# Performance work log

Measured on AMD Instinct MI355X. Metric: run time of the kernel, lower is better.

Reference implementation:

```python
import jax, jax.numpy as jnp
import numpy as np

N = 100000
E = 1600000
D_IN = 64
D_HID = 64
D_OUT = 64


def setup_inputs() -> dict:
    key = jax.random.key(0)
    ks = jax.random.split(key, 12)
    x = jax.random.normal(ks[0], (N, D_IN), dtype=jnp.float32)
    edge_index = jax.random.randint(ks[1], (2, E), 0, N, dtype=jnp.int64)
    s1 = 1.0 / np.sqrt(D_IN)
    s2 = 1.0 / np.sqrt(D_HID)
    return {
        "x": x,
        "edge_index": edge_index,
        "W1l": jax.random.uniform(ks[2], (D_HID, D_IN), jnp.float32, -s1, s1),
        "b1l": jax.random.uniform(ks[3], (D_HID,), jnp.float32, -s1, s1),
        "W1r": jax.random.uniform(ks[4], (D_HID, D_IN), jnp.float32, -s1, s1),
        "W2l": jax.random.uniform(ks[5], (D_HID, D_HID), jnp.float32, -s2, s2),
        "b2l": jax.random.uniform(ks[6], (D_HID,), jnp.float32, -s2, s2),
        "W2r": jax.random.uniform(ks[7], (D_HID, D_HID), jnp.float32, -s2, s2),
        "Wout": jax.random.uniform(ks[8], (D_OUT, D_HID), jnp.float32, -s2, s2),
        "bout": jax.random.uniform(ks[9], (D_OUT,), jnp.float32, -s2, s2),
        "drop": 0,
    }


def _sage_conv(x, src, dst, Wl, bl, Wr, n_nodes):
    # PyG SAGEConv, aggr='mean': out = lin_l(mean_j x_j) + lin_r(x_i)
    msg = x[src]                                            # [E, d] gather
    agg = jax.ops.segment_sum(msg, dst, num_segments=n_nodes)
    deg = jax.ops.segment_sum(jnp.ones((src.shape[0],), x.dtype), dst,
                              num_segments=n_nodes)
    mean = agg / jnp.maximum(deg, 1.0)[:, None]             # empty neighborhoods -> 0
    return mean @ Wl.T + bl + x @ Wr.T


def reference(x, edge_index, W1l, b1l, W1r, W2l, b2l, W2r, Wout, bout, drop):
    src, dst = edge_index[0], edge_index[1]
    n = x.shape[0]
    # dropout is identity in eval mode (training=False); drop unused
    h = jax.nn.relu(_sage_conv(x, src, dst, W1l, b1l, W1r, n))
    h = jax.nn.relu(_sage_conv(h, src, dst, W2l, b2l, W2r, n))
    logits = h @ Wout.T + bout
    return jax.nn.log_softmax(logits, axis=1)
```

## Files before the change

kernel.cpp:

```cpp
#include <hip/hip_runtime.h>


#define TB 256
#define NBINA 256
#define XFB 512
#define CAPB 2560

typedef __attribute__((ext_vector_type(8))) short bf16x8;
typedef __attribute__((ext_vector_type(4))) float f32x4;
typedef __attribute__((ext_vector_type(2))) float f32x2;

__device__ __forceinline__ unsigned short bf16c(float f) {
  union { float f; unsigned u; } v; v.f = f;
  unsigned r = (v.u + 0x7FFFu + ((v.u >> 16) & 1u)) >> 16;
  return (unsigned short)r;
}

__device__ __forceinline__ bf16x8 ld_bf8(const float* p) {
  float4 a = *(const float4*)p;
  float4 b = *(const float4*)(p + 4);
  bf16x8 r;
  r[0] = bf16c(a.x); r[1] = bf16c(a.y); r[2] = bf16c(a.z); r[3] = bf16c(a.w);
  r[4] = bf16c(b.x); r[5] = bf16c(b.y); r[6] = bf16c(b.z); r[7] = bf16c(b.w);
  return r;
}

__device__ __forceinline__ float bflo(unsigned u) { return __uint_as_float(u << 16); }
__device__ __forceinline__ float bfhi(unsigned u) { return __uint_as_float(u & 0xFFFF0000u); }
__device__ __forceinline__ unsigned bfpk(float lo, float hi) {
  return (unsigned)bf16c(lo) | ((unsigned)bf16c(hi) << 16);
}

__global__ __launch_bounds__(256) void k_binA_xf(
    const int* __restrict__ ei, int E,
    int* __restrict__ bucket_fill, unsigned int* __restrict__ bucketData, int NB,
    const float* __restrict__ xin, const float* __restrict__ Wl,
    const float* __restrict__ Wr, const float* __restrict__ bl,
    unsigned short* __restrict__ y, unsigned short* __restrict__ zout, int n) {
  if (blockIdx.x < NBINA) {
    __shared__ int hist[1024];
    __shared__ int base[1024];
    __shared__ int s_nz;
    if (threadIdx.x == 0) s_nz = 0;
    for (int i = threadIdx.x; i < NB; i += TB) hist[i] = 0;
    __syncthreads();
    int nz = 0;
    for (int i = threadIdx.x; i < 2048; i += TB) nz |= ei[2 * i + 1];
    if (nz) atomicOr(&s_nz, 1);
    __syncthreads();
    bool m64 = (s_nz == 0);
    int bb = blockIdx.x;

    long long e0 = (long long)E * bb / NBINA;
    long long e1 = (long long)E * (bb + 1) / NBINA;
    for (long long e = e0 + threadIdx.x; e < e1; e += TB) {
      int dst = m64 ? ((const int2*)ei)[(long long)E + e].x : ei[(long long)E + e];
      atomicAdd(&hist[dst >> 7], 1);
    }
    __syncthreads();
    for (int b = threadIdx.x; b < NB; b += TB) {
      int c = hist[b];
      base[b] = c ? atomicAdd(&bucket_fill[b], c) : 0;
      hist[b] = 0;
    }
    __syncthreads();
    for (long long e = e0 + threadIdx.x; e < e1; e += TB) {
      int src, dst;
      if (m64) {
        src = ((const int2*)ei)[e].x;
        dst = ((const int2*)ei)[(long long)E + e].x;
      } else {
        src = ei[e];
        dst = ei[(long long)E + e];
      }
      int b = dst >> 7;
      int pos = base[b] + atomicAdd(&hist[b], 1);
      if (pos < CAPB)
        bucketData[(size_t)b * CAPB + pos] =
            ((unsigned)(dst & 127) << 24) | (unsigned)src;
    }
    return;
  }

  int lane = threadIdx.x & 63;
  int quad = lane >> 4, m = lane & 15;
  int w0 = ((blockIdx.x - NBINA) * TB + threadIdx.x) >> 6;
  int nw = (XFB * TB) >> 6;

  bf16x8 bfrag[8][2];
  float bias[4];
#pragma unroll
  for (int t = 0; t < 8; ++t) {
    const float* W = (t < 4) ? Wl : Wr;
    int row = (t & 3) * 16 + m;
#pragma unroll
    for (int s = 0; s < 2; ++s)
      bfrag[t][s] = ld_bf8(W + row * 64 + s * 32 + quad * 8);
  }
#pragma unroll
  for (int t = 0; t < 4; ++t) bias[t] = bl[t * 16 + m];

  int nT = (n + 15) >> 4;
  for (int tile = w0; tile < nT; tile += nw) {
    int node0 = tile << 4;
    int mrow = node0 + m;
    if (mrow >= n) mrow = n - 1;
    const float* xr = xin + (size_t)mrow * 64;
    bf16x8 a0 = ld_bf8(xr + quad * 8);
    bf16x8 a1 = ld_bf8(xr + 32 + quad * 8);

    f32x4 acc[8];
#pragma unroll
    for (int t = 0; t < 8; ++t) {
      f32x4 z4 = {0.f, 0.f, 0.f, 0.f};
      z4 = __builtin_amdgcn_mfma_f32_16x16x32_bf16(a0, bfrag[t][0], z4, 0, 0, 0);
      acc[t] = __builtin_amdgcn_mfma_f32_16x16x32_bf16(a1, bfrag[t][1], z4, 0, 0, 0);
    }

#pragma unroll
    for (int r = 0; r < 4; ++r) {
      int node = node0 + quad * 4 + r;
      if (node >= n) break;
      size_t rb = (size_t)node * 64 + m;
#pragma unroll
      for (int t = 0; t < 4; ++t) y[rb + t * 16] = bf16c(acc[t][r]);
#pragma unroll
      for (int t = 0; t < 4; ++t) zout[rb + t * 16] = bf16c(acc[t + 4][r] + bias[t]);
    }
  }
}

__global__ __launch_bounds__(256) void k_binB(
    const unsigned int* __restrict__ bucketData, const int* __restrict__ bucket_fill,
    int* __restrict__ colp, int* __restrict__ cnt) {
  __shared__ unsigned int slice[128 * 64];
  __shared__ int lcnt[128];
  int b = blockIdx.x;
  for (int i = threadIdx.x; i < 128; i += TB) lcnt[i] = 0;
  __syncthreads();
  int fcnt = bucket_fill[b];
  if (fcnt > CAPB) fcnt = CAPB;
  const unsigned int* bd = bucketData + (size_t)b * CAPB;
  for (int k = threadIdx.x; k < fcnt; k += TB) {
    unsigned int rec = bd[k];
    int dl = rec >> 24;
    int pos = atomicAdd(&lcnt[dl], 1);
    if (pos < 64) slice[(dl << 6) + pos] = rec & 0xFFFFFFu;
  }
  __syncthreads();
  size_t obase = (size_t)b * (128 * 64);
  for (int i = threadIdx.x * 4; i < 128 * 64; i += TB * 4) {
    *(uint4*)(colp + obase + i) = *(const uint4*)(slice + i);
  }
  int node0 = b << 7;
  for (int i = threadIdx.x; i < 128; i += TB) cnt[node0 + i] = lcnt[i];
}

__global__ __launch_bounds__(256) void k_xform_b16(
    const unsigned short* zin, const float* __restrict__ Wl,
    const float* __restrict__ Wr, const float* __restrict__ bl,
    unsigned short* __restrict__ y, unsigned short* zout, int n) {
  int lane = threadIdx.x & 63;
  int quad = lane >> 4, m = lane & 15;
  int w0 = (blockIdx.x * blockDim.x + threadIdx.x) >> 6;
  int nw = (gridDim.x * blockDim.x) >> 6;

  bf16x8 bfrag[8][2];
  float bias[4];
#pragma unroll
  for (int t = 0; t < 8; ++t) {
    const float* W = (t < 4) ? Wl : Wr;
    int row = (t & 3) * 16 + m;
#pragma unroll
    for (int s = 0; s < 2; ++s)
      bfrag[t][s] = ld_bf8(W + row * 64 + s * 32 + quad * 8);
  }
#pragma unroll
  for (int t = 0; t < 4; ++t) bias[t] = bl[t * 16 + m];

  int nT = (n + 15) >> 4;
  for (int tile = w0; tile < nT; tile += nw) {
    int node0 = tile << 4;
    int mrow = node0 + m;
    if (mrow >= n) mrow = n - 1;
    const unsigned short* xr = zin + (size_t)mrow * 64;
    bf16x8 a0 = *(const bf16x8*)(xr + quad * 8);
    bf16x8 a1 = *(const bf16x8*)(xr + 32 + quad * 8);

    f32x4 acc[8];
#pragma unroll
    for (int t = 0; t < 8; ++t) {
      f32x4 z4 = {0.f, 0.f, 0.f, 0.f};
      z4 = __builtin_amdgcn_mfma_f32_16x16x32_bf16(a0, bfrag[t][0], z4, 0, 0, 0);
      acc[t] = __builtin_amdgcn_mfma_f32_16x16x32_bf16(a1, bfrag[t][1], z4, 0, 0, 0);
    }

#pragma unroll
    for (int r = 0; r < 4; ++r) {
      int node = node0 + quad * 4 + r;
      if (node >= n) break;
      size_t rb = (size_t)node * 64 + m;
#pragma unroll
      for (int t = 0; t < 4; ++t) y[rb + t * 16] = bf16c(acc[t][r]);
#pragma unroll
      for (int t = 0; t < 4; ++t) zout[rb + t * 16] = bf16c(acc[t + 4][r] + bias[t]);
    }
  }
}

__global__ __launch_bounds__(256) void k_aggr(
    const unsigned short* __restrict__ yb, const int* __restrict__ cnt,
    const int* __restrict__ colp, unsigned short* zio, int n) {
  const unsigned int* y = (const unsigned int*)yb;
  int lane = threadIdx.x & 63;
  int wv = (blockIdx.x * blockDim.x + threadIdx.x) >> 6;
  int g16 = lane & 48;
  int lig = lane & 15;
  int sub = lig >> 3;
  int fo = (lig & 7) * 4;

  int node = (wv << 2) + (g16 >> 4);
  bool act = node < n;
  int cn = act ? node : 0;
  int deg = cnt[cn];
  int jcap = deg < 64 ? deg : 64;
  size_t crow = (size_t)cn << 6;
  int cidxA = colp[crow + lig];
  int cidxB = colp[crow + 16 + lig];

  int wmax = jcap;
  wmax = max(wmax, __shfl_xor(wmax, 16, 64));
  wmax = max(wmax, __shfl_xor(wmax, 32, 64));

  f32x2 acc[4];
#pragma unroll
  for (int k = 0; k < 4; ++k) acc[k] = (f32x2){0.f, 0.f};

#define ACCUM(U)                                             \
  do {                                                       \
    acc[0] += (f32x2){bflo((U).x), bfhi((U).x)};             \
    acc[1] += (f32x2){bflo((U).y), bfhi((U).y)};             \
    acc[2] += (f32x2){bflo((U).z), bfhi((U).z)};             \
    acc[3] += (f32x2){bflo((U).w), bfhi((U).w)};             \
  } while (0)

#pragma unroll
  for (int s = 0; s < 16; s += 2) {
    int slot = s + sub;
    int c = __shfl(cidxA, g16 | slot, 64);
    if (slot < jcap) {
      uint4 v = *(const uint4*)(y + ((size_t)c << 5) + fo);
      ACCUM(v);
    }
  }
  if (wmax > 16) {
#pragma unroll
    for (int s = 0; s < 16; s += 2) {
      int slot = s + sub;
      int c = __shfl(cidxB, g16 | slot, 64);
      if (slot + 16 < jcap) {
        uint4 v = *(const uint4*)(y + ((size_t)c << 5) + fo);
        ACCUM(v);
      }
    }
  }
  if (wmax > 32) {
    int cidxC = colp[crow + 32 + lig];
    int cidxD = colp[crow + 48 + lig];
    {
      int lim = (wmax < 48 ? wmax : 48) - 32;
      for (int s = 0; s < lim; s += 2) {
        int slot = s + sub;
        int c = __shfl(cidxC, g16 | slot, 64);
        if (slot + 32 < jcap) {
          uint4 v = *(const uint4*)(y + ((size_t)c << 5) + fo);
          ACCUM(v);
        }
      }
    }
    if (wmax > 48) {
      int lim = wmax - 48;
      for (int s = 0; s < lim; s += 2) {
        int slot = s + sub;
        int c = __shfl(cidxD, g16 | slot, 64);
        if (slot + 48 < jcap) {
          uint4 v = *(const uint4*)(y + ((size_t)c << 5) + fo);
          ACCUM(v);
        }
      }
    }
  }
#undef ACCUM

#pragma unroll
  for (int k = 0; k < 4; ++k) {
    acc[k].x += __shfl_xor(acc[k].x, 8, 64);
    acc[k].y += __shfl_xor(acc[k].y, 8, 64);
  }

  if (act && sub == 0) {
    float inv = (deg > 0) ? 1.0f / (float)deg : 0.f;
    unsigned int* zp = (unsigned int*)(zio + ((size_t)node << 6)) + fo;
    uint4 zv = *(uint4*)zp;
    zv.x = bfpk(fmaxf(fmaf(acc[0].x, inv, bflo(zv.x)), 0.f),
                fmaxf(fmaf(acc[0].y, inv, bfhi(zv.x)), 0.f));
    zv.y = bfpk(fmaxf(fmaf(acc[1].x, inv, bflo(zv.y)), 0.f),
                fmaxf(fmaf(acc[1].y, inv, bfhi(zv.y)), 0.f));
    zv.z = bfpk(fmaxf(fmaf(acc[2].x, inv, bflo(zv.z)), 0.f),
                fmaxf(fmaf(acc[2].y, inv, bfhi(zv.z)), 0.f));
    zv.w = bfpk(fmaxf(fmaf(acc[3].x, inv, bflo(zv.w)), 0.f),
                fmaxf(fmaf(acc[3].y, inv, bfhi(zv.w)), 0.f));
    *(uint4*)zp = zv;
  }
}

__global__ __launch_bounds__(256) void k_out(
    const unsigned short* __restrict__ h, const float* __restrict__ Wo,
    const float* __restrict__ bo, float* __restrict__ out, int n) {
  int lane = threadIdx.x & 63;
  int quad = lane >> 4, m = lane & 15;
  int w0 = (blockIdx.x * blockDim.x + threadIdx.x) >> 6;
  int nw = (gridDim.x * blockDim.x) >> 6;

  bf16x8 bfrag[4][2];
  float bias[4];
#pragma unroll
  for (int t = 0; t < 4; ++t) {
    int row = t * 16 + m;
#pragma unroll
    for (int s = 0; s < 2; ++s)
      bfrag[t][s] = ld_bf8(Wo + row * 64 + s * 32 + quad * 8);
    bias[t] = bo[t * 16 + m];
  }

  int nT = (n + 15) >> 4;
  for (int tile = w0; tile < nT; tile += nw) {
    int node0 = tile << 4;
    int mrow = node0 + m;
    if (mrow >= n) mrow = n - 1;
    const unsigned short* xr = h + (size_t)mrow * 64;
    bf16x8 a0 = *(const bf16x8*)(xr + quad * 8);
    bf16x8 a1 = *(const bf16x8*)(xr + 32 + quad * 8);

    f32x4 acc[4];
#pragma unroll
    for (int t = 0; t < 4; ++t) {
      f32x4 z4 = {0.f, 0.f, 0.f, 0.f};
      z4 = __builtin_amdgcn_mfma_f32_16x16x32_bf16(a0, bfrag[t][0], z4, 0, 0, 0);
      acc[t] = __builtin_amdgcn_mfma_f32_16x16x32_bf16(a1, bfrag[t][1], z4, 0, 0, 0);
    }

#pragma unroll
    for (int r = 0; r < 4; ++r) {
      int node = node0 + quad * 4 + r;
      if (node >= n) break;
      float l0 = acc[0][r] + bias[0];
      float l1 = acc[1][r] + bias[1];
      float l2 = acc[2][r] + bias[2];
      float l3 = acc[3][r] + bias[3];
      float mx = fmaxf(fmaxf(l0, l1), fmaxf(l2, l3));
#pragma unroll
      for (int off = 1; off <= 8; off <<= 1) mx = fmaxf(mx, __shfl_xor(mx, off, 64));
      float s = expf(l0 - mx) + expf(l1 - mx) + expf(l2 - mx) + expf(l3 - mx);
#pragma unroll
      for (int off = 1; off <= 8; off <<= 1) s += __shfl_xor(s, off, 64);
      float ls = logf(s);
      size_t rb = (size_t)node * 64 + m;
      out[rb + 0]  = l0 - mx - ls;
      out[rb + 16] = l1 - mx - ls;
      out[rb + 32] = l2 - mx - ls;
      out[rb + 48] = l3 - mx - ls;
    }
  }
}

extern "C" void kernel_launch(void* const* d_in, const int* in_sizes, int n_in,
                              void* d_out, int out_size, void* d_ws, size_t ws_size,
                              hipStream_t stream) {
  const float* x    = (const float*)d_in[0];
  const int*   ei   = (const int*)d_in[1];
  const float* W1l  = (const float*)d_in[2];
  const float* b1l  = (const float*)d_in[3];
  const float* W1r  = (const float*)d_in[4];
  const float* W2l  = (const float*)d_in[5];
  const float* b2l  = (const float*)d_in[6];
  const float* W2r  = (const float*)d_in[7];
  const float* Wout = (const float*)d_in[8];
  const float* bout = (const float*)d_in[9];
  int N = in_sizes[0] / 64;
  int E = in_sizes[1] / 2;
  int NB = (N + 127) >> 7;

  char* p = (char*)d_ws;
  auto carve = [&](size_t bytes) {
    char* r = p;
    p += (bytes + 255) & ~(size_t)255;
    return r;
  };
  int* bucket_fill   = (int*)carve((size_t)NB * 4);
  int* cnt           = (int*)carve((size_t)NB * 128 * 4);
  int* colp          = (int*)carve((size_t)NB * 128 * 64 * 4);
  unsigned short* y  = (unsigned short*)carve((size_t)N * 64 * 2);
  unsigned short* z  = (unsigned short*)carve((size_t)N * 64 * 2);
  unsigned int* bucketData = (unsigned int*)carve((size_t)NB * CAPB * 4);

  hipMemsetAsync(bucket_fill, 0, (size_t)NB * 4, stream);

  int aggr_blocks = (N + 15) / 16;
  k_binA_xf<<<NBINA + XFB, TB, 0, stream>>>(ei, E, bucket_fill, bucketData, NB,
                                            x, W1l, W1r, b1l, y, z, N);
  k_binB<<<NB, TB, 0, stream>>>(bucketData, bucket_fill, colp, cnt);
  k_aggr<<<aggr_blocks, TB, 0, stream>>>(y, cnt, colp, z, N);
  k_xform_b16<<<XFB, TB, 0, stream>>>(z, W2l, W2r, b2l, y, z, N);
  k_aggr<<<aggr_blocks, TB, 0, stream>>>(y, cnt, colp, z, N);
  k_out<<<XFB, TB, 0, stream>>>(z, Wout, bout, (float*)d_out, N);
}
```

Baseline: 243.4 us.

## Bin edges into per-block fixed-capacity cells instead of global bucket atomics

The edge-binning pass now writes each source block's edges into a private fixed-size cell per destination bucket, replacing the two-pass histogram plus global atomic reservation. This removes one pass over the edge list, the global atomics and the memset. The second pass now has each thread read one cell serially. Cells are capped at 32 entries, so overflow can silently drop edges under skewed degree, and per-thread serial reads in k_binB may coalesce poorly.

```diff
diff --git a/kernel.cpp b/kernel.cpp
--- a/kernel.cpp
+++ b/kernel.cpp
@@ -4,7 +4,8 @@
 #define TB 256
 #define NBINA 256
 #define XFB 512
-#define CAPB 2560
+#define CAPC 32
+#define NBPAD 1024
 
 typedef __attribute__((ext_vector_type(8))) short bf16x8;
 typedef __attribute__((ext_vector_type(4))) float f32x4;
@@ -33,16 +34,15 @@
 
 __global__ __launch_bounds__(256) void k_binA_xf(
     const int* __restrict__ ei, int E,
-    int* __restrict__ bucket_fill, unsigned int* __restrict__ bucketData, int NB,
+    int* __restrict__ cellcnt, unsigned int* __restrict__ bucketData, int NB,
     const float* __restrict__ xin, const float* __restrict__ Wl,
     const float* __restrict__ Wr, const float* __restrict__ bl,
     unsigned short* __restrict__ y, unsigned short* __restrict__ zout, int n) {
   if (blockIdx.x < NBINA) {
-    __shared__ int hist[1024];
-    __shared__ int base[1024];
+    __shared__ int lcnt[NBPAD];
     __shared__ int s_nz;
     if (threadIdx.x == 0) s_nz = 0;
-    for (int i = threadIdx.x; i < NB; i += TB) hist[i] = 0;
+    for (int i = threadIdx.x; i < NBPAD; i += TB) lcnt[i] = 0;
     __syncthreads();
     int nz = 0;
     for (int i = threadIdx.x; i < 2048; i += TB) nz |= ei[2 * i + 1];
@@ -53,17 +53,6 @@
 
     long long e0 = (long long)E * bb / NBINA;
     long long e1 = (long long)E * (bb + 1) / NBINA;
-    for (long long e = e0 + threadIdx.x; e < e1; e += TB) {
-      int dst = m64 ? ((const int2*)ei)[(long long)E + e].x : ei[(long long)E + e];
-      atomicAdd(&hist[dst >> 7], 1);
-    }
-    __syncthreads();
-    for (int b = threadIdx.x; b < NB; b += TB) {
-      int c = hist[b];
-      base[b] = c ? atomicAdd(&bucket_fill[b], c) : 0;
-      hist[b] = 0;
-    }
-    __syncthreads();
     for (long long e = e0 + threadIdx.x; e < e1; e += TB) {
       int src, dst;
       if (m64) {
@@ -74,11 +63,13 @@
         dst = ei[(long long)E + e];
       }
       int b = dst >> 7;
-      int pos = base[b] + atomicAdd(&hist[b], 1);
-      if (pos < CAPB)
-        bucketData[(size_t)b * CAPB + pos] =
+      int pos = atomicAdd(&lcnt[b], 1);
+      if (pos < CAPC)
+        bucketData[((size_t)b * NBINA + bb) * CAPC + pos] =
             ((unsigned)(dst & 127) << 24) | (unsigned)src;
     }
+    __syncthreads();
+    for (int b = threadIdx.x; b < NB; b += TB) cellcnt[bb * NBPAD + b] = lcnt[b];
     return;
   }
 
@@ -131,18 +122,18 @@
 }
 
 __global__ __launch_bounds__(256) void k_binB(
-    const unsigned int* __restrict__ bucketData, const int* __restrict__ bucket_fill,
+    const unsigned int* __restrict__ bucketData, const int* __restrict__ cellcnt,
     int* __restrict__ colp, int* __restrict__ cnt) {
   __shared__ unsigned int slice[128 * 64];
   __shared__ int lcnt[128];
   int b = blockIdx.x;
   for (int i = threadIdx.x; i < 128; i += TB) lcnt[i] = 0;
   __syncthreads();
-  int fcnt = bucket_fill[b];
-  if (fcnt > CAPB) fcnt = CAPB;
-  const unsigned int* bd = bucketData + (size_t)b * CAPB;
-  for (int k = threadIdx.x; k < fcnt; k += TB) {
-    unsigned int rec = bd[k];
+  int c = cellcnt[threadIdx.x * NBPAD + b];
+  if (c > CAPC) c = CAPC;
+  const unsigned int* cell = bucketData + ((size_t)b * NBINA + threadIdx.x) * CAPC;
+  for (int k = 0; k < c; ++k) {
+    unsigned int rec = cell[k];
     int dl = rec >> 24;
     int pos = atomicAdd(&lcnt[dl], 1);
     if (pos < 64) slice[(dl << 6) + pos] = rec & 0xFFFFFFu;
@@ -397,19 +388,17 @@
     p += (bytes + 255) & ~(size_t)255;
     return r;
   };
-  int* bucket_fill   = (int*)carve((size_t)NB * 4);
+  int* cellcnt       = (int*)carve((size_t)NBINA * NBPAD * 4);
   int* cnt           = (int*)carve((size_t)NB * 128 * 4);
   int* colp          = (int*)carve((size_t)NB * 128 * 64 * 4);
   unsigned short* y  = (unsigned short*)carve((size_t)N * 64 * 2);
   unsigned short* z  = (unsigned short*)carve((size_t)N * 64 * 2);
-  unsigned int* bucketData = (unsigned int*)carve((size_t)NB * CAPB * 4);
-
-  hipMemsetAsync(bucket_fill, 0, (size_t)NB * 4, stream);
+  unsigned int* bucketData = (unsigned int*)carve((size_t)NB * NBINA * CAPC * 4);
 
   int aggr_blocks = (N + 15) / 16;
-  k_binA_xf<<<NBINA + XFB, TB, 0, stream>>>(ei, E, bucket_fill, bucketData, NB,
+  k_binA_xf<<<NBINA + XFB, TB, 0, stream>>>(ei, E, cellcnt, bucketData, NB,
                                             x, W1l, W1r, b1l, y, z, N);
-  k_binB<<<NB, TB, 0, stream>>>(bucketData, bucket_fill, colp, cnt);
+  k_binB<<<NB, TB, 0, stream>>>(bucketData, cellcnt, colp, cnt);
   k_aggr<<<aggr_blocks, TB, 0, stream>>>(y, cnt, colp, z, N);
   k_xform_b16<<<XFB, TB, 0, stream>>>(z, W2l, W2r, b2l, y, z, N);
   k_aggr<<<aggr_blocks, TB, 0, stream>>>(y, cnt, colp, z, N);
```

After: 239.9 us. About the same (-1.5%).
